# Kernel optimization log

Measured on AMD Instinct MI355X. Metric: run time of the kernel, lower is better.

## Reference

```python
import jax, jax.numpy as jnp
import numpy as np

NUM_TOKENS = 8192
HIDDEN = 4096
NUM_EXPERTS = 64
TOP_K = 8


def setup_inputs() -> dict:
    key = jax.random.key(0)
    k1, k2, k3 = jax.random.split(key, 3)
    tokens = jax.random.normal(k1, (NUM_TOKENS, HIDDEN), dtype=jnp.float32)
    token_probs = jax.random.uniform(k2, (NUM_TOKENS, NUM_EXPERTS), dtype=jnp.float32)
    # exactly TOP_K experts per token -> static num_out_tokens
    scores = jax.random.normal(k3, (NUM_TOKENS, NUM_EXPERTS))
    _, topk_idx = jax.lax.top_k(scores, TOP_K)  # [T, K]
    rows = jnp.arange(NUM_TOKENS)[:, None]
    routing_map = jnp.zeros((NUM_TOKENS, NUM_EXPERTS), dtype=bool).at[rows, topk_idx].set(True)
    return {
        "tokens": tokens,
        "token_probs": token_probs,
        "routing_map": routing_map,
        "num_out_tokens": NUM_TOKENS * TOP_K,
    }


def reference(tokens, token_probs, routing_map, num_out_tokens):
    # Fallback (non-fused) path of TurboTokenPermuter.forward.
    num_tokens, _ = tokens.shape
    # routing_map.bool().T -> [E, T]; masked_select in row-major order =
    # for each expert (in order), the token ids routed to it (in token order).
    flat_mask = routing_map.T.reshape(-1)  # [E*T]
    # stable argsort of ~mask puts flat positions of True entries first, in order
    perm = jnp.argsort(~flat_mask, stable=True)[:num_out_tokens]  # flat E*T indices
    sorted_indices = (perm % num_tokens).astype(jnp.int32)  # token ids (column index)
    permuted_probs = token_probs.T.reshape(-1)[perm]
    permuted_input = tokens[sorted_indices]  # index_select along dim 0
    return permuted_input, permuted_probs, sorted_indices
```

## Files before the change

kernel.cpp:

```cpp
#include <hip/hip_runtime.h>
#include <stdint.h>

#define NTOK   8192
#define NEXP   64
#define HID    4096
#define TOPK   8
#define OUTROW 65536
#define CHUNK  256
#define NCHUNK 32
#define NPART  2048

typedef float f32x4 __attribute__((ext_vector_type(4)));
typedef unsigned long long u64;

__global__ void mask_count_kernel(const int* __restrict__ map,
                                  u64* __restrict__ masks,
                                  int* __restrict__ pcnt) {
    int c = blockIdx.x;
    int tid = threadIdx.x;
    int w = tid >> 6, lane = tid & 63;

    __shared__ u64 sm[CHUNK];
    __shared__ int hcnt[NEXP];
    if (tid < NEXP) hcnt[tid] = 0;

    int t0 = c * CHUNK + w * 64;
#pragma unroll 8
    for (int i = 0; i < 64; ++i) {
        int v = map[(size_t)(t0 + i) * NEXP + lane];
        u64 bal = __ballot(v != 0);
        if (lane == 0) sm[w * 64 + i] = bal;
    }
    __syncthreads();

    u64 mk = sm[tid];
    masks[c * CHUNK + tid] = mk;
    while (mk) {
        int e = __ffsll((long long)mk) - 1;
        atomicAdd(&hcnt[e], 1);
        mk &= mk - 1;
    }
    __syncthreads();
    if (tid < NEXP) pcnt[tid * NCHUNK + c] = hcnt[tid];
}

__global__ void scan_kernel(const int* __restrict__ pcnt, int* __restrict__ poffs) {
    __shared__ int s[256];
    int tid = threadIdx.x;
    int v[8];
    int sum = 0;
#pragma unroll
    for (int i = 0; i < 8; ++i) { v[i] = pcnt[tid * 8 + i]; sum += v[i]; }
    s[tid] = sum;
    __syncthreads();
    for (int off = 1; off < 256; off <<= 1) {
        int x = (tid >= off) ? s[tid - off] : 0;
        __syncthreads();
        s[tid] += x;
        __syncthreads();
    }
    int base = (tid == 0) ? 0 : s[tid - 1];
#pragma unroll
    for (int i = 0; i < 8; ++i) { poffs[tid * 8 + i] = base; base += v[i]; }
}

__global__ void mega_kernel(const u64* __restrict__ masks,
                            const float* __restrict__ probs,
                            const int* __restrict__ poffs,
                            const float* __restrict__ tokens,
                            float* __restrict__ out_rows,
                            float* __restrict__ out_probs,
                            float* __restrict__ out_idx) {
    int t = blockIdx.x;
    int c = t >> 8, tin = t & 255;
    int tid = threadIdx.x;

    const f32x4* sp = (const f32x4*)(tokens + (size_t)t * HID);
    f32x4 v0 = __builtin_nontemporal_load(sp + tid);
    f32x4 v1 = __builtin_nontemporal_load(sp + tid + 256);
    f32x4 v2 = __builtin_nontemporal_load(sp + tid + 512);
    f32x4 v3 = __builtin_nontemporal_load(sp + tid + 768);

    __shared__ u64 red[256];
    __shared__ int s_pos[TOPK];

    u64 mk = masks[t];
    int e[TOPK];
    u64 tmp = mk;
#pragma unroll
    for (int j = 0; j < TOPK; ++j) {
        e[j] = tmp ? (__ffsll((long long)tmp) - 1) : 0;
        tmp &= tmp - 1;
    }

    u64 contrib = 0;
    if (tid < tin) {
        u64 mi = masks[c * CHUNK + tid];
#pragma unroll
        for (int j = 0; j < TOPK; ++j)
            contrib |= ((mi >> e[j]) & 1ull) << (8 * j);
    }
    red[tid] = contrib;
    __syncthreads();
    for (int off = 128; off > 0; off >>= 1) {
        if (tid < off) red[tid] += red[tid + off];
        __syncthreads();
    }
    u64 ranks = red[0];

    if (tid < TOPK) {
        int ej = e[tid];
        int pos = poffs[ej * NCHUNK + c] + (int)((ranks >> (8 * tid)) & 0xff);
        if ((unsigned)pos >= OUTROW) pos = 0;
        s_pos[tid] = pos;
        out_idx[pos] = (float)t;
        out_probs[pos] = probs[(size_t)t * NEXP + ej];
    }
    __syncthreads();

#pragma unroll
    for (int j = 0; j < TOPK; ++j) {
        int p = s_pos[j];
        f32x4* dp = (f32x4*)(out_rows + (size_t)p * HID);
        dp[tid]       = v0;
        dp[tid + 256] = v1;
        dp[tid + 512] = v2;
        dp[tid + 768] = v3;
    }
}

extern "C" void kernel_launch(void* const* d_in, const int* in_sizes, int n_in,
                              void* d_out, int out_size, void* d_ws, size_t ws_size,
                              hipStream_t stream) {
    const float* tokens = (const float*)d_in[0];
    const float* probs  = (const float*)d_in[1];
    const int*   map    = (const int*)d_in[2];

    float* out_rows  = (float*)d_out;
    float* out_probs = out_rows + (size_t)OUTROW * HID;
    float* out_idx   = out_probs + OUTROW;

    u64* masks = (u64*)d_ws;
    int* pcnt  = (int*)(masks + NTOK);
    int* poffs = pcnt + NPART;

    mask_count_kernel<<<NCHUNK, CHUNK, 0, stream>>>(map, masks, pcnt);
    scan_kernel<<<1, CHUNK, 0, stream>>>(pcnt, poffs);
    mega_kernel<<<NTOK, CHUNK, 0, stream>>>(masks, probs, poffs, tokens,
                                            out_rows, out_probs, out_idx);
}
```

Before: 276.2 us.

## Precompute per-token expert ranks in mask kernel, drop per-block reduction

The first kernel now computes, for every token, its within-chunk rank for each of its selected experts. It does this with a per-lane prefix count over the ballot masks plus per-wave totals, and packs the ranks into a u64 per token. The copy kernel then reads the packed rank and no longer runs the shared-memory tree reduction and its barriers in each of the 8192 blocks. Row stores also become nontemporal and are grouped by vector slot. This adds a 32 KB shared array and a serial 64-step scan to the small first kernel.

After: 271.2 us. About the same (-1.8%).

```diff
diff --git a/kernel.cpp b/kernel.cpp
--- a/kernel.cpp
+++ b/kernel.cpp
@@ -13,16 +13,17 @@
 typedef float f32x4 __attribute__((ext_vector_type(4)));
 typedef unsigned long long u64;
 
-__global__ void mask_count_kernel(const int* __restrict__ map,
-                                  u64* __restrict__ masks,
-                                  int* __restrict__ pcnt) {
+__global__ void mask_rank_kernel(const int* __restrict__ map,
+                                 u64* __restrict__ masks,
+                                 u64* __restrict__ tok_rank,
+                                 int* __restrict__ pcnt) {
     int c = blockIdx.x;
     int tid = threadIdx.x;
     int w = tid >> 6, lane = tid & 63;
 
     __shared__ u64 sm[CHUNK];
-    __shared__ int hcnt[NEXP];
-    if (tid < NEXP) hcnt[tid] = 0;
+    __shared__ unsigned short rnk[CHUNK][NEXP];
+    __shared__ int wtot[4][NEXP];
 
     int t0 = c * CHUNK + w * 64;
 #pragma unroll 8
@@ -33,15 +34,35 @@
     }
     __syncthreads();
 
+    int cnt = 0;
+#pragma unroll 8
+    for (int i = 0; i < 64; ++i) {
+        u64 mk = sm[w * 64 + i];
+        rnk[w * 64 + i][lane] = (unsigned short)cnt;
+        cnt += (int)((mk >> lane) & 1ull);
+    }
+    wtot[w][lane] = cnt;
+    __syncthreads();
+
     u64 mk = sm[tid];
     masks[c * CHUNK + tid] = mk;
-    while (mk) {
-        int e = __ffsll((long long)mk) - 1;
-        atomicAdd(&hcnt[e], 1);
-        mk &= mk - 1;
+    int myw = tid >> 6;
+    u64 tmp = mk;
+    u64 packed = 0;
+#pragma unroll
+    for (int j = 0; j < TOPK; ++j) {
+        int e = tmp ? (__ffsll((long long)tmp) - 1) : 0;
+        tmp &= tmp - 1;
+        int r = rnk[tid][e];
+        if (myw > 0) r += wtot[0][e];
+        if (myw > 1) r += wtot[1][e];
+        if (myw > 2) r += wtot[2][e];
+        packed |= (u64)(r & 0xff) << (8 * j);
     }
-    __syncthreads();
-    if (tid < NEXP) pcnt[tid * NCHUNK + c] = hcnt[tid];
+    tok_rank[c * CHUNK + tid] = packed;
+
+    if (tid < NEXP)
+        pcnt[tid * NCHUNK + c] = wtot[0][tid] + wtot[1][tid] + wtot[2][tid] + wtot[3][tid];
 }
 
 __global__ void scan_kernel(const int* __restrict__ pcnt, int* __restrict__ poffs) {
@@ -65,6 +86,7 @@
 }
 
 __global__ void mega_kernel(const u64* __restrict__ masks,
+                            const u64* __restrict__ tok_rank,
                             const float* __restrict__ probs,
                             const int* __restrict__ poffs,
                             const float* __restrict__ tokens,
@@ -72,7 +94,7 @@
                             float* __restrict__ out_probs,
                             float* __restrict__ out_idx) {
     int t = blockIdx.x;
-    int c = t >> 8, tin = t & 255;
+    int c = t >> 8;
     int tid = threadIdx.x;
 
     const f32x4* sp = (const f32x4*)(tokens + (size_t)t * HID);
@@ -81,52 +103,32 @@
     f32x4 v2 = __builtin_nontemporal_load(sp + tid + 512);
     f32x4 v3 = __builtin_nontemporal_load(sp + tid + 768);
 
-    __shared__ u64 red[256];
-    __shared__ int s_pos[TOPK];
+    u64 mk = masks[t];
+    u64 rk = tok_rank[t];
 
-    u64 mk = masks[t];
-    int e[TOPK];
+    f32x4* dp[TOPK];
     u64 tmp = mk;
 #pragma unroll
     for (int j = 0; j < TOPK; ++j) {
-        e[j] = tmp ? (__ffsll((long long)tmp) - 1) : 0;
+        int e = tmp ? (__ffsll((long long)tmp) - 1) : 0;
         tmp &= tmp - 1;
+        int pos = poffs[e * NCHUNK + c] + (int)((rk >> (8 * j)) & 0xff);
+        if ((unsigned)pos >= OUTROW) pos = 0;
+        dp[j] = (f32x4*)(out_rows + (size_t)pos * HID);
+        if (tid == j) {
+            out_idx[pos] = (float)t;
+            out_probs[pos] = probs[(size_t)t * NEXP + e];
+        }
     }
 
-    u64 contrib = 0;
-    if (tid < tin) {
-        u64 mi = masks[c * CHUNK + tid];
 #pragma unroll
-        for (int j = 0; j < TOPK; ++j)
-            contrib |= ((mi >> e[j]) & 1ull) << (8 * j);
-    }
-    red[tid] = contrib;
-    __syncthreads();
-    for (int off = 128; off > 0; off >>= 1) {
-        if (tid < off) red[tid] += red[tid + off];
-        __syncthreads();
-    }
-    u64 ranks = red[0];
-
-    if (tid < TOPK) {
-        int ej = e[tid];
-        int pos = poffs[ej * NCHUNK + c] + (int)((ranks >> (8 * tid)) & 0xff);
-        if ((unsigned)pos >= OUTROW) pos = 0;
-        s_pos[tid] = pos;
-        out_idx[pos] = (float)t;
-        out_probs[pos] = probs[(size_t)t * NEXP + ej];
-    }
-    __syncthreads();
-
+    for (int j = 0; j < TOPK; ++j) __builtin_nontemporal_store(v0, dp[j] + tid);
 #pragma unroll
-    for (int j = 0; j < TOPK; ++j) {
-        int p = s_pos[j];
-        f32x4* dp = (f32x4*)(out_rows + (size_t)p * HID);
-        dp[tid]       = v0;
-        dp[tid + 256] = v1;
-        dp[tid + 512] = v2;
-        dp[tid + 768] = v3;
-    }
+    for (int j = 0; j < TOPK; ++j) __builtin_nontemporal_store(v1, dp[j] + tid + 256);
+#pragma unroll
+    for (int j = 0; j < TOPK; ++j) __builtin_nontemporal_store(v2, dp[j] + tid + 512);
+#pragma unroll
+    for (int j = 0; j < TOPK; ++j) __builtin_nontemporal_store(v3, dp[j] + tid + 768);
 }
 
 extern "C" void kernel_launch(void* const* d_in, const int* in_sizes, int n_in,
@@ -140,12 +142,13 @@
     float* out_probs = out_rows + (size_t)OUTROW * HID;
     float* out_idx   = out_probs + OUTROW;
 
-    u64* masks = (u64*)d_ws;
-    int* pcnt  = (int*)(masks + NTOK);
-    int* poffs = pcnt + NPART;
+    u64* masks    = (u64*)d_ws;
+    u64* tok_rank = masks + NTOK;
+    int* pcnt     = (int*)(tok_rank + NTOK);
+    int* poffs    = pcnt + NPART;
 
-    mask_count_kernel<<<NCHUNK, CHUNK, 0, stream>>>(map, masks, pcnt);
+    mask_rank_kernel<<<NCHUNK, CHUNK, 0, stream>>>(map, masks, tok_rank, pcnt);
     scan_kernel<<<1, CHUNK, 0, stream>>>(pcnt, poffs);
-    mega_kernel<<<NTOK, CHUNK, 0, stream>>>(masks, probs, poffs, tokens,
+    mega_kernel<<<NTOK, CHUNK, 0, stream>>>(masks, tok_rank, probs, poffs, tokens,
                                             out_rows, out_probs, out_idx);
 }
```

## Restructure permute as per-(chunk,expert) gather with contiguous output writes

Applied to the files above, without the earlier changes.

Replaces the per-token scatter kernel, which read each token row once and wrote it to 8 scattered output rows, with a per-(chunk,expert) kernel. Each block ranks the routed tokens with a ballot and popcount, then gathers their rows into a contiguous output segment using nontemporal stores. This drops the per-token 256-wide rank reduction and makes the writes sequential. In exchange each token row is now read 8 times (relying on L2/MALL hits), and block work varies with expert load.

After: 317.3 us. +14.9%, slower.

```diff
diff --git a/kernel.cpp b/kernel.cpp
--- a/kernel.cpp
+++ b/kernel.cpp
@@ -64,68 +64,70 @@
     for (int i = 0; i < 8; ++i) { poffs[tid * 8 + i] = base; base += v[i]; }
 }
 
-__global__ void mega_kernel(const u64* __restrict__ masks,
-                            const float* __restrict__ probs,
-                            const int* __restrict__ poffs,
-                            const float* __restrict__ tokens,
-                            float* __restrict__ out_rows,
-                            float* __restrict__ out_probs,
-                            float* __restrict__ out_idx) {
-    int t = blockIdx.x;
-    int c = t >> 8, tin = t & 255;
+__global__ void seg_kernel(const u64* __restrict__ masks,
+                           const float* __restrict__ probs,
+                           const int* __restrict__ poffs,
+                           const float* __restrict__ tokens,
+                           float* __restrict__ out_rows,
+                           float* __restrict__ out_probs,
+                           float* __restrict__ out_idx) {
+    int blk = blockIdx.x;
+    int c = blk >> 6, e = blk & 63;
     int tid = threadIdx.x;
+    int w = tid >> 6, lane = tid & 63;
 
-    const f32x4* sp = (const f32x4*)(tokens + (size_t)t * HID);
-    f32x4 v0 = __builtin_nontemporal_load(sp + tid);
-    f32x4 v1 = __builtin_nontemporal_load(sp + tid + 256);
-    f32x4 v2 = __builtin_nontemporal_load(sp + tid + 512);
-    f32x4 v3 = __builtin_nontemporal_load(sp + tid + 768);
+    __shared__ int s_src[CHUNK];
+    __shared__ int wcnt[4];
 
-    __shared__ u64 red[256];
-    __shared__ int s_pos[TOPK];
+    int t = c * CHUNK + tid;
+    u64 mk = masks[t];
+    bool m = (mk >> e) & 1ull;
+    u64 bal = __ballot(m);
+    int rank = __popcll(bal & ((1ull << lane) - 1ull));
+    if (lane == 0) wcnt[w] = __popcll(bal);
+    __syncthreads();
+    int wbase = 0;
+#pragma unroll
+    for (int i = 0; i < 4; ++i) wbase += (i < w) ? wcnt[i] : 0;
+    int total = wcnt[0] + wcnt[1] + wcnt[2] + wcnt[3];
+    int base = poffs[e * NCHUNK + c];
 
-    u64 mk = masks[t];
-    int e[TOPK];
-    u64 tmp = mk;
-#pragma unroll
-    for (int j = 0; j < TOPK; ++j) {
-        e[j] = tmp ? (__ffsll((long long)tmp) - 1) : 0;
-        tmp &= tmp - 1;
-    }
-
-    u64 contrib = 0;
-    if (tid < tin) {
-        u64 mi = masks[c * CHUNK + tid];
-#pragma unroll
-        for (int j = 0; j < TOPK; ++j)
-            contrib |= ((mi >> e[j]) & 1ull) << (8 * j);
-    }
-    red[tid] = contrib;
-    __syncthreads();
-    for (int off = 128; off > 0; off >>= 1) {
-        if (tid < off) red[tid] += red[tid + off];
-        __syncthreads();
-    }
-    u64 ranks = red[0];
-
-    if (tid < TOPK) {
-        int ej = e[tid];
-        int pos = poffs[ej * NCHUNK + c] + (int)((ranks >> (8 * tid)) & 0xff);
-        if ((unsigned)pos >= OUTROW) pos = 0;
-        s_pos[tid] = pos;
+    if (m) {
+        int local = wbase + rank;
+        s_src[local] = t;
+        int pos = base + local;
         out_idx[pos] = (float)t;
-        out_probs[pos] = probs[(size_t)t * NEXP + ej];
+        out_probs[pos] = probs[(size_t)t * NEXP + e];
     }
     __syncthreads();
 
-#pragma unroll
-    for (int j = 0; j < TOPK; ++j) {
-        int p = s_pos[j];
-        f32x4* dp = (f32x4*)(out_rows + (size_t)p * HID);
-        dp[tid]       = v0;
-        dp[tid + 256] = v1;
-        dp[tid + 512] = v2;
-        dp[tid + 768] = v3;
+    int i = 0;
+    for (; i + 2 <= total; i += 2) {
+        int s0 = s_src[i], s1 = s_src[i + 1];
+        const f32x4* sp0 = (const f32x4*)(tokens + (size_t)s0 * HID);
+        const f32x4* sp1 = (const f32x4*)(tokens + (size_t)s1 * HID);
+        f32x4* dp0 = (f32x4*)(out_rows + (size_t)(base + i) * HID);
+        f32x4* dp1 = (f32x4*)(out_rows + (size_t)(base + i + 1) * HID);
+        f32x4 a0 = sp0[tid], a1 = sp0[tid + 256], a2 = sp0[tid + 512], a3 = sp0[tid + 768];
+        f32x4 b0 = sp1[tid], b1 = sp1[tid + 256], b2 = sp1[tid + 512], b3 = sp1[tid + 768];
+        __builtin_nontemporal_store(a0, dp0 + tid);
+        __builtin_nontemporal_store(a1, dp0 + tid + 256);
+        __builtin_nontemporal_store(a2, dp0 + tid + 512);
+        __builtin_nontemporal_store(a3, dp0 + tid + 768);
+        __builtin_nontemporal_store(b0, dp1 + tid);
+        __builtin_nontemporal_store(b1, dp1 + tid + 256);
+        __builtin_nontemporal_store(b2, dp1 + tid + 512);
+        __builtin_nontemporal_store(b3, dp1 + tid + 768);
+    }
+    if (i < total) {
+        int s0 = s_src[i];
+        const f32x4* sp0 = (const f32x4*)(tokens + (size_t)s0 * HID);
+        f32x4* dp0 = (f32x4*)(out_rows + (size_t)(base + i) * HID);
+        f32x4 a0 = sp0[tid], a1 = sp0[tid + 256], a2 = sp0[tid + 512], a3 = sp0[tid + 768];
+        __builtin_nontemporal_store(a0, dp0 + tid);
+        __builtin_nontemporal_store(a1, dp0 + tid + 256);
+        __builtin_nontemporal_store(a2, dp0 + tid + 512);
+        __builtin_nontemporal_store(a3, dp0 + tid + 768);
     }
 }
 
@@ -146,6 +148,6 @@
 
     mask_count_kernel<<<NCHUNK, CHUNK, 0, stream>>>(map, masks, pcnt);
     scan_kernel<<<1, CHUNK, 0, stream>>>(pcnt, poffs);
-    mega_kernel<<<NTOK, CHUNK, 0, stream>>>(masks, probs, poffs, tokens,
+    seg_kernel<<<NPART, CHUNK, 0, stream>>>(masks, probs, poffs, tokens,
                                             out_rows, out_probs, out_idx);
 }
```
